# Kernel tuning notes

Measured on AMD Instinct MI355X. Metric: run time of the kernel, lower is better.

The kernel has to match this reference:

```python
import jax, jax.numpy as jnp
import numpy as np

B, T, H = 32, 4096, 128   # batch, seq len, feature dim (ctor L=128)
N = 128                    # S5 state size (S5(dim, dim))
DEPTH = 2                  # L_LT
D_OUT = 64                 # adaptive pool output length (ctor D)
LN_EPS = 1e-5


def setup_inputs() -> dict:
    key = jax.random.key(0)
    ks = iter(jax.random.split(key, 40))
    def nrm(shape, s):
        return (jax.random.normal(next(ks), shape, jnp.float32) * s).astype(jnp.float32)
    inp = {}
    inp['x'] = jax.random.normal(next(ks), (B, T, H), jnp.float32)
    # LayerNorm params (stacked over depth)
    inp['ln1_g'] = jnp.ones((DEPTH, H), jnp.float32)
    inp['ln1_b'] = jnp.zeros((DEPTH, H), jnp.float32)
    inp['ln2_g'] = jnp.ones((DEPTH, H), jnp.float32)
    inp['ln2_b'] = jnp.zeros((DEPTH, H), jnp.float32)
    # S5 params: diagonal complex Lambda, complex B/C, real D skip, per-state log step
    inp['Lam_re'] = -0.5 * jnp.ones((DEPTH, N), jnp.float32)
    inp['Lam_im'] = jnp.tile(jnp.pi * jnp.arange(N, dtype=jnp.float32), (DEPTH, 1))
    inp['B_re'] = nrm((DEPTH, N, H), 1.0 / np.sqrt(H))
    inp['B_im'] = nrm((DEPTH, N, H), 1.0 / np.sqrt(H))
    inp['C_re'] = nrm((DEPTH, H, N), 1.0 / np.sqrt(N))
    inp['C_im'] = nrm((DEPTH, H, N), 1.0 / np.sqrt(N))
    inp['D_skip'] = nrm((DEPTH, H), 1.0)
    inp['log_step'] = jax.random.uniform(next(ks), (DEPTH, N), jnp.float32,
                                         minval=np.log(1e-3), maxval=np.log(1e-1))
    # MLP params
    inp['W1'] = nrm((DEPTH, H, 2 * H), 1.0 / np.sqrt(H))
    inp['b1'] = jnp.zeros((DEPTH, 2 * H), jnp.float32)
    inp['W2'] = nrm((DEPTH, 2 * H, H), 1.0 / np.sqrt(2 * H))
    inp['b2'] = jnp.zeros((DEPTH, H), jnp.float32)
    # Conv1d params (out_ch, in_ch, k=5)
    cs = 1.0 / np.sqrt(H * 5)
    inp['conv1_w'] = nrm((H, H, 5), cs)
    inp['conv1_b'] = jnp.zeros((H,), jnp.float32)
    inp['conv2_w'] = nrm((H, H, 5), cs)
    inp['conv2_b'] = jnp.zeros((H,), jnp.float32)
    return inp


def _layer_norm(x, g, b):
    mu = jnp.mean(x, axis=-1, keepdims=True)
    var = jnp.mean(jnp.square(x - mu), axis=-1, keepdims=True)
    return (x - mu) * jax.lax.rsqrt(var + LN_EPS) * g + b


def _s5(u, lam_re, lam_im, b_re, b_im, c_re, c_im, d_skip, log_step):
    # u: [B, T, H] real. Diagonal S5 with ZOH discretization + parallel scan.
    lam = lam_re + 1j * lam_im                       # (N,) complex
    dt = jnp.exp(log_step)                           # (N,)
    lam_bar = jnp.exp(lam * dt)                      # (N,)
    Bc = b_re + 1j * b_im                            # (N, H)
    B_bar = ((lam_bar - 1.0) / lam)[:, None] * Bc    # (N, H)
    Bu = jnp.einsum('bth,nh->btn', u.astype(jnp.complex64), B_bar)  # [B,T,N]
    A = jnp.broadcast_to(lam_bar.astype(jnp.complex64), Bu.shape)
    def binop(e1, e2):
        a1, x1 = e1
        a2, x2 = e2
        return a1 * a2, a2 * x1 + x2
    _, xs = jax.lax.associative_scan(binop, (A, Bu), axis=1)        # [B,T,N]
    Cc = c_re + 1j * c_im                            # (H, N)
    y = 2.0 * jnp.real(jnp.einsum('btn,hn->bth', xs, Cc)) + u * d_skip
    return y


def _conv1d_s2(x, w, b):
    # x: [B, C, L]; stride 2, padding 2, kernel 5
    y = jax.lax.conv_general_dilated(x, w, window_strides=(2,), padding=[(2, 2)],
                                     dimension_numbers=('NCH', 'OIH', 'NCH'))
    return y + b[None, :, None]


def reference(x, ln1_g, ln1_b, ln2_g, ln2_b, Lam_re, Lam_im, B_re, B_im,
              C_re, C_im, D_skip, log_step, W1, b1, W2, b2,
              conv1_w, conv1_b, conv2_w, conv2_b):
    for i in range(DEPTH):
        # S5 sub-block
        res = x
        xn = _layer_norm(x, ln1_g[i], ln1_b[i])
        x = res + _s5(xn, Lam_re[i], Lam_im[i], B_re[i], B_im[i],
                      C_re[i], C_im[i], D_skip[i], log_step[i])
        # MLP sub-block (dropout = identity in eval)
        res = x
        xn = _layer_norm(x, ln2_g[i], ln2_b[i])
        h = jax.nn.gelu(jnp.einsum('bth,hf->btf', xn, W1[i]) + b1[i], approximate=False)
        x = res + jnp.einsum('btf,fh->bth', h, W2[i]) + b2[i]
    x = jnp.transpose(x, (0, 2, 1))                  # [B, H, T]
    x = jax.nn.relu(_conv1d_s2(x, conv1_w, conv1_b))  # [B, H, T/2]
    x = jax.nn.relu(_conv1d_s2(x, conv2_w, conv2_b))  # [B, H, T/4]
    Lin = x.shape[-1]
    # AdaptiveAvgPool1d(D_OUT): Lin divisible by D_OUT -> uniform windows
    x = x.reshape(x.shape[0], x.shape[1], D_OUT, Lin // D_OUT).mean(axis=-1)
    return x  # [B, H, D_OUT]
```

## Files before the change

kernel.cpp:

```cpp
#include <hip/hip_runtime.h>
#include <math.h>

#define BATCH 32
#define TSEQ  4096
#define HD    128
#define NST   128
#define BT    (BATCH*TSEQ)
#define LC    64
#define NCHK  (TSEQ/LC)

typedef unsigned short bf16;
typedef __attribute__((ext_vector_type(8))) short bf16x8;
typedef __attribute__((ext_vector_type(4))) float f32x4;

__device__ inline float bf2f(bf16 s) {
    union { unsigned int u; float f; } v; v.u = ((unsigned int)s) << 16; return v.f;
}
__device__ inline bf16 f2bf(float f) {
    union { float f; unsigned int u; } v; v.f = f;
    unsigned int u = v.u;
    unsigned int r = (u + 0x7fffu + ((u >> 16) & 1u)) >> 16;
    return (bf16)r;
}
__device__ inline unsigned int pkpair(float lo, float hi) {
    union { float f; unsigned int u; } a, b;
    a.f = lo; b.f = hi;
    return __builtin_amdgcn_perm(b.u + 0x8000u, a.u + 0x8000u, 0x07060302u);
}
__device__ inline bf16x8 pack8f(float4 f0, float4 f1) {
    union { bf16x8 v; unsigned int u[4]; } t;
    t.u[0] = pkpair(f0.x, f0.y);
    t.u[1] = pkpair(f0.z, f0.w);
    t.u[2] = pkpair(f1.x, f1.y);
    t.u[3] = pkpair(f1.z, f1.w);
    return t.v;
}
__device__ inline float2 cmul2(float2 a, float2 b) {
    return make_float2(a.x*b.x - a.y*b.y, a.x*b.y + a.y*b.x);
}
__device__ inline float gelu_f(float x) {
    float u = x*(0.7978845608f + 0.0356774081f*x*x);
    return __fdividef(x, 1.f + __expf(-2.f*u));
}
__device__ inline float2 upk(unsigned int w) {
    union { unsigned int u; float f; } a, b;
    a.u = w << 16; b.u = w & 0xffff0000u;
    return make_float2(a.f, b.f);
}
__device__ inline unsigned int pk(float2 x) { return pkpair(x.x, x.y); }

__global__ void prep_s5(const float* __restrict__ Lam_re, const float* __restrict__ Lam_im,
                        const float* __restrict__ B_re,  const float* __restrict__ B_im,
                        const float* __restrict__ C_re,  const float* __restrict__ C_im,
                        const float* __restrict__ log_step,
                        const float* __restrict__ ln1_g, const float* __restrict__ ln1_b,
                        const float* __restrict__ D_skip,
                        bf16* __restrict__ Wbu_bf,
                        bf16* __restrict__ Wc_bf,
                        float* __restrict__ Sb, float* __restrict__ biasb,
                        float* __restrict__ gd, float* __restrict__ bd,
                        float4* __restrict__ coefs,
                        float2* __restrict__ apow)
{
    int i = blockIdx.x, n = threadIdx.x;
    int in = i*NST + n;
    float lr = Lam_re[in], li = Lam_im[in];
    float dt = expf(log_step[in]);
    float ea = expf(lr*dt);
    float ar = ea*cosf(li*dt), ai = ea*sinf(li*dt);
    float xx = ar - 1.f, yy = ai;
    float den = lr*lr + li*li;
    float sr = (xx*lr + yy*li)/den;
    float si = (yy*lr - xx*li)/den;
    float2 a2 = make_float2(ar, ai);
    float2 p = a2;
    float2* apr = apow + (size_t)i*64*128;
    for (int j = 0; j < 64; ++j) {
        apr[n*64 + j] = p;
        p = cmul2(p, a2);
    }
    float2 q = a2;
    #pragma unroll
    for (int t = 0; t < 6; ++t) q = cmul2(q, q);
    coefs[in] = make_float4(ar, ai, q.x, q.y);

    const float* g  = ln1_g + i*HD;
    const float* bb = ln1_b + i*HD;
    const float* br = B_re + (size_t)in*HD;
    const float* bi = B_im + (size_t)in*HD;
    bf16* wb = Wbu_bf + (size_t)i*256*128;
    float s_re = 0.f, s_im = 0.f, bc_re = 0.f, bc_im = 0.f;
    for (int h = 0; h < HD; ++h) {
        float wre = sr*br[h] - si*bi[h];
        float wim = sr*bi[h] + si*br[h];
        bf16 wrb = f2bf(g[h]*wre), wib = f2bf(g[h]*wim);
        wb[(2*n)*128 + h]   = wrb;
        wb[(2*n+1)*128 + h] = wib;
        s_re += bf2f(wrb); s_im += bf2f(wib);
        bc_re += bb[h]*wre; bc_im += bb[h]*wim;
    }
    Sb[i*256 + 2*n] = s_re;     Sb[i*256 + 2*n+1] = s_im;
    biasb[i*256 + 2*n] = bc_re; biasb[i*256 + 2*n+1] = bc_im;

    const float* cr = C_re + (size_t)i*HD*NST;
    const float* ci = C_im + (size_t)i*HD*NST;
    bf16* wc = Wc_bf + (size_t)i*128*256;
    for (int h = 0; h < HD; ++h) {
        wc[h*256 + 2*n]   = f2bf( 2.f * cr[h*NST + n]);
        wc[h*256 + 2*n+1] = f2bf(-2.f * ci[h*NST + n]);
    }
    gd[i*HD + n] = g[n]*D_skip[i*HD + n];
    bd[i*HD + n] = bb[n]*D_skip[i*HD + n];
}

__global__ void prep_w1(const float* __restrict__ W1, const float* __restrict__ b1,
                        const float* __restrict__ ln2_g, const float* __restrict__ ln2_b,
                        bf16* __restrict__ W1_bf, float* __restrict__ S1,
                        float* __restrict__ bias1p)
{
    int i = blockIdx.x, f = threadIdx.x;
    const float* g  = ln2_g + i*HD;
    const float* bb = ln2_b + i*HD;
    bf16* w = W1_bf + (size_t)i*256*128;
    int j = ((f >> 5) << 5) | (((f >> 2) & 1) << 4) | (((f >> 3) & 3) << 2) | (f & 3);
    float S = 0.f, bi_ = b1[i*256 + f];
    for (int h = 0; h < HD; ++h) {
        float wv = W1[(size_t)i*32768 + h*256 + f];
        bf16 wbv = f2bf(g[h]*wv);
        w[j*128 + h] = wbv;
        S += bf2f(wbv);
        bi_ += bb[h]*wv;
    }
    S1[i*256 + f] = S;
    bias1p[i*256 + f] = bi_;
}

__global__ void prep_w2(const float* __restrict__ W2, bf16* __restrict__ W2_bf)
{
    int i = blockIdx.x, h = threadIdx.x;
    bf16* w = W2_bf + (size_t)i*128*256;
    for (int f = 0; f < 256; ++f)
        w[h*256 + f] = f2bf(W2[(size_t)i*32768 + f*128 + h]);
}

__global__ void prep_wB(const float* __restrict__ w1, const float* __restrict__ w2,
                        bf16* __restrict__ wB1, bf16* __restrict__ wB2)
{
    int idx = blockIdx.x*256 + threadIdx.x;
    if (idx >= 163840) return;
    const float* w = (idx < 81920) ? w1 : w2;
    bf16* wb       = (idx < 81920) ? wB1 : wB2;
    int r   = idx % 81920;
    int c   = r / 640;
    int tap = (r % 640) / 128;
    int ic  = r % 128;
    wb[r] = f2bf(w[(c*128 + ic)*5 + tap]);
}

template<typename TA>
__global__ __launch_bounds__(512, 2) void lngemm2(
    const TA* __restrict__ A,
    const bf16* __restrict__ Bt,
    const float* __restrict__ Svec, const float* __restrict__ bvec,
    bf16* __restrict__ outB,
    float2* __restrict__ munrs)
{
    __shared__ bf16 Bs[256*136];
    __shared__ float Sl[256], bl[256];

    int tid = threadIdx.x;
    #pragma unroll
    for (int it = 0; it < 8; ++it) {
        int f = it*512 + tid;
        int n = f >> 4, kk = (f & 15)*8;
        *(bf16x8*)&Bs[n*136 + kk] = *(const bf16x8*)(Bt + n*128 + kk);
    }
    if (tid < 256) { Sl[tid] = Svec[tid]; bl[tid] = bvec[tid]; }
    __syncthreads();

    int wid = tid >> 6, lane = tid & 63;
    int quad = lane >> 4, cl = lane & 15;
    int s0 = blockIdx.x*16 + wid*2;
    size_t row0 = (size_t)s0*16 + cl;

    bf16x8 af[2][4];
    float mu[2], rs[2], mr[2];
    #pragma unroll
    for (int p = 0; p < 2; ++p) {
        size_t row = row0 + (size_t)p*16;
        float sm = 0.f, sq = 0.f;
        if constexpr (sizeof(TA) == 2) {
            const bf16* ar = (const bf16*)A + row*128;
            #pragma unroll
            for (int ks = 0; ks < 4; ++ks) {
                af[p][ks] = *(const bf16x8*)(ar + quad*8 + ks*32);
                union { bf16x8 v; unsigned int u[4]; } aa; aa.v = af[p][ks];
                #pragma unroll
                for (int jp = 0; jp < 4; ++jp) {
                    float2 vv = upk(aa.u[jp]);
                    sm += vv.x + vv.y;
                    sq += vv.x*vv.x + vv.y*vv.y;
                }
            }
        } else {
            const float* ar = (const float*)A + row*128;
            #pragma unroll
            for (int ks = 0; ks < 4; ++ks) {
                float4 f0 = *(const float4*)(ar + quad*8 + ks*32);
                float4 f1 = *(const float4*)(ar + quad*8 + ks*32 + 4);
                sm += f0.x + f0.y + f0.z + f0.w + f1.x + f1.y + f1.z + f1.w;
                sq += f0.x*f0.x + f0.y*f0.y + f0.z*f0.z + f0.w*f0.w
                    + f1.x*f1.x + f1.y*f1.y + f1.z*f1.z + f1.w*f1.w;
                af[p][ks] = pack8f(f0, f1);
            }
        }
        sm += __shfl_xor(sm, 16); sm += __shfl_xor(sm, 32);
        sq += __shfl_xor(sq, 16); sq += __shfl_xor(sq, 32);
        mu[p] = sm * (1.f/128.f);
        rs[p] = rsqrtf(sq*(1.f/128.f) - mu[p]*mu[p] + 1e-5f);
        mr[p] = mu[p]*rs[p];
        if (quad == 0) munrs[row] = make_float2(mu[p], rs[p]);
    }

    #pragma unroll
    for (int g = 0; g < 4; ++g) {
        f32x4 acc0[4] = {}, acc1[4] = {};
        #pragma unroll
        for (int t4 = 0; t4 < 4; ++t4) {
            const bf16* wrp = &Bs[(((g*4+t4)*16) + cl)*136 + quad*8];
            #pragma unroll
            for (int ks = 0; ks < 4; ++ks) {
                bf16x8 w = *(const bf16x8*)(wrp + ks*32);
                acc0[t4] = __builtin_amdgcn_mfma_f32_16x16x32_bf16(w, af[0][ks], acc0[t4], 0, 0, 0);
                acc1[t4] = __builtin_amdgcn_mfma_f32_16x16x32_bf16(w, af[1][ks], acc1[t4], 0, 0, 0);
            }
        }
        #pragma unroll
        for (int t4 = 0; t4 < 4; ++t4) {
            int n0 = (g*4+t4)*16 + quad*4;
            float4 S4 = *(const float4*)&Sl[n0];
            float4 b4 = *(const float4*)&bl[n0];
            float4 o;
            o.x = rs[0]*acc0[t4][0] - mr[0]*S4.x + b4.x;
            o.y = rs[0]*acc0[t4][1] - mr[0]*S4.y + b4.y;
            o.z = rs[0]*acc0[t4][2] - mr[0]*S4.z + b4.z;
            o.w = rs[0]*acc0[t4][3] - mr[0]*S4.w + b4.w;
            *(uint2*)(outB + row0*256 + n0) = make_uint2(pkpair(o.x, o.y), pkpair(o.z, o.w));
            o.x = rs[1]*acc1[t4][0] - mr[1]*S4.x + b4.x;
            o.y = rs[1]*acc1[t4][1] - mr[1]*S4.y + b4.y;
            o.z = rs[1]*acc1[t4][2] - mr[1]*S4.z + b4.z;
            o.w = rs[1]*acc1[t4][3] - mr[1]*S4.w + b4.w;
            *(uint2*)(outB + (row0+16)*256 + n0) = make_uint2(pkpair(o.x, o.y), pkpair(o.z, o.w));
        }
    }
}

template<typename TR>
__global__ __launch_bounds__(512, 2) void gemm2s(
    const bf16* __restrict__ A,
    const bf16* __restrict__ Bt,
    bf16* out,
    const TR* resid,
    const float2* __restrict__ munrs,
    const float* __restrict__ gdp, const float* __restrict__ bdp,
    const float2* __restrict__ carry,
    const float2* __restrict__ apow)
{
    __shared__ bf16 Bs[128*264];
    __shared__ float gdl[128], bdl[128];

    int tid = threadIdx.x;
    #pragma unroll
    for (int it = 0; it < 8; ++it) {
        int f = it*512 + tid;
        int n = f >> 5, kk = (f & 31)*8;
        *(bf16x8*)&Bs[n*264 + kk] = *(const bf16x8*)(Bt + n*256 + kk);
    }
    if (tid < 128) { gdl[tid] = gdp[tid]; bdl[tid] = bdp[tid]; }
    __syncthreads();

    int wid = tid >> 6, lane = tid & 63;
    int quad = lane >> 4, cl = lane & 15;
    int s0 = blockIdx.x*16 + wid*2;
    size_t row0 = (size_t)s0*16 + cl;

    bf16x8 af[2][8];
    float mu[2], rs[2];
    #pragma unroll
    for (int p = 0; p < 2; ++p) {
        size_t row = row0 + (size_t)p*16;
        float2 m2 = munrs[row]; mu[p] = m2.x; rs[p] = m2.y;
        const bf16* ar = A + row*256 + quad*8;
        int b  = (int)(row >> 12);
        int tp = (int)(row & 4095);
        int cc = tp >> 6, j = tp & 63;
        const float2* cin = carry + (size_t)cc*(BATCH*NST) + (size_t)b*NST;
        const float2* ap  = apow + j;
        #pragma unroll
        for (int ks = 0; ks < 8; ++ks) {
            union { bf16x8 v; unsigned int u[4]; } t;
            t.v = *(const bf16x8*)(ar + ks*32);
            int n0 = quad*4 + ks*16;
            #pragma unroll
            for (int jp = 0; jp < 4; ++jp) {
                float2 v  = upk(t.u[jp]);
                float2 ad = cmul2(ap[(size_t)(n0+jp)*64], cin[n0+jp]);
                t.u[jp] = pk(make_float2(v.x + ad.x, v.y + ad.y));
            }
            af[p][ks] = t.v;
        }
    }

    ushort4 rvh[2][8];
    if constexpr (sizeof(TR) == 2) {
        #pragma unroll
        for (int p = 0; p < 2; ++p)
            #pragma unroll
            for (int nt = 0; nt < 8; ++nt)
                rvh[p][nt] = *(const ushort4*)((const bf16*)resid
                               + (row0 + (size_t)p*16)*128 + nt*16 + quad*4);
    }

    #pragma unroll
    for (int nt = 0; nt < 8; ++nt) {
        const bf16* wrp = &Bs[(nt*16 + cl)*264 + quad*8];
        f32x4 a0 = {}, a1 = {};
        #pragma unroll
        for (int ks = 0; ks < 8; ++ks) {
            bf16x8 w = *(const bf16x8*)(wrp + ks*32);
            a0 = __builtin_amdgcn_mfma_f32_16x16x32_bf16(w, af[0][ks], a0, 0, 0, 0);
            a1 = __builtin_amdgcn_mfma_f32_16x16x32_bf16(w, af[1][ks], a1, 0, 0, 0);
        }
        int n0 = nt*16 + quad*4;
        float4 g4 = *(const float4*)&gdl[n0];
        float4 b4 = *(const float4*)&bdl[n0];
        #pragma unroll
        for (int p = 0; p < 2; ++p) {
            f32x4 ac = p ? a1 : a0;
            size_t oidx = (row0 + (size_t)p*16)*128 + n0;
            float4 rv;
            if constexpr (sizeof(TR) == 2) {
                ushort4 u4 = rvh[p][nt];
                rv = make_float4(bf2f(u4.x), bf2f(u4.y), bf2f(u4.z), bf2f(u4.w));
            } else {
                rv = *(const float4*)((const float*)resid + oidx);
            }
            float4 o;
            o.x = rv.x + ac[0] + (rv.x - mu[p])*rs[p]*g4.x + b4.x;
            o.y = rv.y + ac[1] + (rv.y - mu[p])*rs[p]*g4.y + b4.y;
            o.z = rv.z + ac[2] + (rv.z - mu[p])*rs[p]*g4.z + b4.z;
            o.w = rv.w + ac[3] + (rv.w - mu[p])*rs[p]*g4.w + b4.w;
            *(uint2*)(out + oidx) = make_uint2(pkpair(o.x, o.y), pkpair(o.z, o.w));
        }
    }
}

__global__ __launch_bounds__(1024, 2) void mlp_fused(
    const bf16* X,
    const bf16* __restrict__ W1t,
    const bf16* __restrict__ W2t,
    const float* __restrict__ S1v, const float* __restrict__ b1v,
    const float* __restrict__ b2v,
    bf16* out)
{
    __shared__ bf16 As1[256*136];
    __shared__ bf16 Bs2[128*264];
    __shared__ float S1l[256], b1l[256], b2l[128];

    int tid = threadIdx.x;
    #pragma unroll
    for (int it = 0; it < 4; ++it) {
        int f = it*1024 + tid;
        int n = f >> 4, kk = (f & 15)*8;
        *(bf16x8*)&As1[n*136 + kk] = *(const bf16x8*)(W1t + n*128 + kk);
    }
    #pragma unroll
    for (int it = 0; it < 4; ++it) {
        int f = it*1024 + tid;
        int n = f >> 5, kk = (f & 31)*8;
        *(bf16x8*)&Bs2[n*264 + kk] = *(const bf16x8*)(W2t + n*256 + kk);
    }
    if (tid < 256)      { S1l[tid] = S1v[tid]; b1l[tid] = b1v[tid]; }
    else if (tid < 384) { int h = tid - 256; b2l[h] = b2v[h]; }
    __syncthreads();

    int wid = tid >> 6, lane = tid & 63;
    int quad = lane >> 4, cl = lane & 15;
    int s = blockIdx.x*16 + wid;
    size_t row = (size_t)s*16 + cl;

    const bf16* ar = X + row*128;
    bf16x8 af[4];
    float sm = 0.f, sq = 0.f;
    #pragma unroll
    for (int ks = 0; ks < 4; ++ks) {
        af[ks] = *(const bf16x8*)(ar + quad*8 + ks*32);
        union { bf16x8 v; unsigned int u[4]; } aa; aa.v = af[ks];
        #pragma unroll
        for (int jp = 0; jp < 4; ++jp) {
            float2 vv = upk(aa.u[jp]);
            sm += vv.x + vv.y;
            sq += vv.x*vv.x + vv.y*vv.y;
        }
    }
    sm += __shfl_xor(sm, 16); sm += __shfl_xor(sm, 32);
    sq += __shfl_xor(sq, 16); sq += __shfl_xor(sq, 32);
    float mu = sm * (1.f/128.f);
    float rs = rsqrtf(sq*(1.f/128.f) - mu*mu + 1e-5f);
    float mr = mu*rs;

    union { unsigned int u[16][2]; bf16x8 v[8]; } hp;
    #pragma unroll
    for (int half = 0; half < 2; ++half) {
        f32x4 acc[8] = {};
        #pragma unroll
        for (int nt = 0; nt < 8; ++nt) {
            const bf16* wrp = &As1[(((half*8+nt)*16) + cl)*136 + quad*8];
            #pragma unroll
            for (int ks = 0; ks < 4; ++ks)
                acc[nt] = __builtin_amdgcn_mfma_f32_16x16x32_bf16(
                              *(const bf16x8*)(wrp + ks*32), af[ks], acc[nt], 0, 0, 0);
        }
        #pragma unroll
        for (int nt = 0; nt < 8; ++nt) {
            int NT = half*8 + nt;
            int fb = ((NT >> 1) << 5) + (quad << 3) + ((NT & 1) << 2);
            float4 S4 = *(const float4*)&S1l[fb];
            float4 b4 = *(const float4*)&b1l[fb];
            float4 o;
            o.x = gelu_f(rs*acc[nt][0] - mr*S4.x + b4.x);
            o.y = gelu_f(rs*acc[nt][1] - mr*S4.y + b4.y);
            o.z = gelu_f(rs*acc[nt][2] - mr*S4.z + b4.z);
            o.w = gelu_f(rs*acc[nt][3] - mr*S4.w + b4.w);
            hp.u[NT][0] = pkpair(o.x, o.y);
            hp.u[NT][1] = pkpair(o.z, o.w);
        }
    }

    #pragma unroll
    for (int nt = 0; nt < 8; ++nt) {
        const bf16* wrp = &Bs2[(nt*16 + cl)*264 + quad*8];
        f32x4 a0 = {};
        #pragma unroll
        for (int ks = 0; ks < 8; ++ks) {
            bf16x8 w = *(const bf16x8*)(wrp + ks*32);
            a0 = __builtin_amdgcn_mfma_f32_16x16x32_bf16(w, hp.v[ks], a0, 0, 0, 0);
        }
        int n0 = nt*16 + quad*4;
        size_t oidx = row*128 + n0;
        float4 b4 = *(const float4*)&b2l[n0];
        ushort4 u4 = *(const ushort4*)(X + oidx);
        float4 o;
        o.x = a0[0] + b4.x + bf2f(u4.x);
        o.y = a0[1] + b4.y + bf2f(u4.y);
        o.z = a0[2] + b4.z + bf2f(u4.z);
        o.w = a0[3] + b4.w + bf2f(u4.w);
        *(uint2*)(out + oidx) = make_uint2(pkpair(o.x, o.y), pkpair(o.z, o.w));
    }
}

__global__ __launch_bounds__(256) void scan_local(uint2* __restrict__ xs,
                                                  const float4* __restrict__ coefs,
                                                  float2* __restrict__ carry)
{
    int flat = blockIdx.x*256 + threadIdx.x;
    int n2 = flat & 63;
    int b = (flat >> 6) & 31;
    int c = flat >> 11;
    float4 cf0 = coefs[2*n2], cf1 = coefs[2*n2+1];
    float2 a0 = make_float2(cf0.x, cf0.y);
    float2 a1 = make_float2(cf1.x, cf1.y);
    uint2* base = xs + ((size_t)(b*TSEQ + c*LC))*64 + n2;
    float2 x0 = make_float2(0.f, 0.f), x1 = make_float2(0.f, 0.f);
    uint2 v = base[0];
    #pragma unroll 4
    for (int j = 0; j < LC; ++j) {
        uint2 vc = v;
        if (j + 1 < LC) v = base[(size_t)(j+1)*64];
        float2 v0 = upk(vc.x), v1 = upk(vc.y);
        x0 = make_float2(a0.x*x0.x - a0.y*x0.y + v0.x, a0.x*x0.y + a0.y*x0.x + v0.y);
        x1 = make_float2(a1.x*x1.x - a1.y*x1.y + v1.x, a1.x*x1.y + a1.y*x1.x + v1.y);
        base[(size_t)j*64] = make_uint2(pk(x0), pk(x1));
    }
    carry[c*(BATCH*NST) + b*NST + 2*n2]   = x0;
    carry[c*(BATCH*NST) + b*NST + 2*n2+1] = x1;
}

__global__ void scan_carry(float2* __restrict__ carry, const float4* __restrict__ coefs)
{
    int flat = blockIdx.x*256 + threadIdx.x;
    int n = flat & 127;
    float4 cf = coefs[n];
    float2 aL = make_float2(cf.z, cf.w);
    float2 x = make_float2(0.f, 0.f);
    for (int c = 0; c < NCHK; ++c) {
        float2* p = carry + c*(BATCH*NST) + flat;
        float2 v = *p;
        *p = x;
        x = make_float2(aL.x*x.x - aL.y*x.y + v.x, aL.x*x.y + aL.y*x.x + v.y);
    }
}

__global__ __launch_bounds__(256, 4) void conv1_mfma(
    const bf16* __restrict__ X,
    const bf16* __restrict__ wB,
    const float* __restrict__ bias,
    bf16* __restrict__ out,
    int Tin, int Lout)
{
    __shared__ bf16 As[128][72];
    __shared__ bf16 Bs[128][72];
    int tid  = threadIdx.x;
    int lane = tid & 63;
    int wave = tid >> 6;
    int wm = wave >> 1, wn = wave & 1;
    int quad = lane >> 4, cl = lane & 15;
    int row0 = blockIdx.x * 128;
    int b  = row0 / Lout;
    int l0 = row0 % Lout;
    const bf16* Xb = X + (size_t)b*Tin*128;

    f32x4 acc[4][4] = {};

    for (int k0 = 0; k0 < 640; k0 += 64) {
        int tap = k0 / 128;
        int icb = k0 % 128;
        #pragma unroll
        for (int it = 0; it < 4; ++it) {
            int idx = it*256 + tid;
            int r = idx >> 3, kof = (idx & 7) * 8;
            int t = 2*(l0 + r) - 2 + tap;
            bf16x8 z = {0,0,0,0,0,0,0,0};
            if (t >= 0 && t < Tin) z = *(const bf16x8*)(Xb + (size_t)t*128 + icb + kof);
            *(bf16x8*)&As[r][kof] = z;
        }
        #pragma unroll
        for (int it = 0; it < 4; ++it) {
            int idx = it*256 + tid;
            int n = idx >> 3, kof = (idx & 7) * 8;
            *(bf16x8*)&Bs[n][kof] = *(const bf16x8*)(wB + (size_t)n*640 + k0 + kof);
        }
        __syncthreads();
        #pragma unroll
        for (int kk = 0; kk < 64; kk += 32) {
            bf16x8 af[4], bfr[4];
            #pragma unroll
            for (int i = 0; i < 4; ++i)
                af[i] = *(const bf16x8*)&As[wm*64 + i*16 + cl][kk + quad*8];
            #pragma unroll
            for (int j = 0; j < 4; ++j)
                bfr[j] = *(const bf16x8*)&Bs[wn*64 + j*16 + cl][kk + quad*8];
            #pragma unroll
            for (int i = 0; i < 4; ++i)
                #pragma unroll
                for (int j = 0; j < 4; ++j)
                    acc[i][j] = __builtin_amdgcn_mfma_f32_16x16x32_bf16(
                                    bfr[j], af[i], acc[i][j], 0, 0, 0);
        }
        __syncthreads();
    }

    #pragma unroll
    for (int i = 0; i < 4; ++i) {
        int grow = row0 + wm*64 + i*16 + cl;
        #pragma unroll
        for (int j = 0; j < 4; ++j) {
            int gcol = wn*64 + j*16 + quad*4;
            float4 bv = *(const float4*)(bias + gcol);
            float4 t;
            t.x = fmaxf(acc[i][j][0] + bv.x, 0.f); t.y = fmaxf(acc[i][j][1] + bv.y, 0.f);
            t.z = fmaxf(acc[i][j][2] + bv.z, 0.f); t.w = fmaxf(acc[i][j][3] + bv.w, 0.f);
            uint2 pu = make_uint2(pkpair(t.x, t.y), pkpair(t.z, t.w));
            *(uint2*)(out + (size_t)grow*128 + gcol) = pu;
        }
    }
}

__global__ __launch_bounds__(256, 4) void conv2_pool(
    const bf16* __restrict__ X,
    const bf16* __restrict__ wB,
    const float* __restrict__ bias,
    float* __restrict__ outp,
    int Tin, int Lout)
{
    __shared__ bf16 As[128][72];
    __shared__ bf16 Bs[128][72];
    int tid  = threadIdx.x;
    int lane = tid & 63;
    int wave = tid >> 6;
    int wm = wave >> 1, wn = wave & 1;
    int quad = lane >> 4, cl = lane & 15;
    int row0 = blockIdx.x * 128;
    int b  = row0 / Lout;
    int l0 = row0 % Lout;
    int d0 = l0 / 16;
    const bf16* Xb = X + (size_t)b*Tin*128;

    f32x4 acc[4][4] = {};

    for (int k0 = 0; k0 < 640; k0 += 64) {
        int tap = k0 / 128;
        int icb = k0 % 128;
        #pragma unroll
        for (int it = 0; it < 4; ++it) {
            int idx = it*256 + tid;
            int r = idx >> 3, kof = (idx & 7) * 8;
            int t = 2*(l0 + r) - 2 + tap;
            bf16x8 z = {0,0,0,0,0,0,0,0};
            if (t >= 0 && t < Tin) z = *(const bf16x8*)(Xb + (size_t)t*128 + icb + kof);
            *(bf16x8*)&As[r][kof] = z;
        }
        #pragma unroll
        for (int it = 0; it < 4; ++it) {
            int idx = it*256 + tid;
            int n = idx >> 3, kof = (idx & 7) * 8;
            *(bf16x8*)&Bs[n][kof] = *(const bf16x8*)(wB + (size_t)n*640 + k0 + kof);
        }
        __syncthreads();
        #pragma unroll
        for (int kk = 0; kk < 64; kk += 32) {
            bf16x8 af[4], bfr[4];
            #pragma unroll
            for (int i = 0; i < 4; ++i)
                af[i] = *(const bf16x8*)&As[wm*64 + i*16 + cl][kk + quad*8];
            #pragma unroll
            for (int j = 0; j < 4; ++j)
                bfr[j] = *(const bf16x8*)&Bs[wn*64 + j*16 + cl][kk + quad*8];
            #pragma unroll
            for (int i = 0; i < 4; ++i)
                #pragma unroll
                for (int j = 0; j < 4; ++j)
                    acc[i][j] = __builtin_amdgcn_mfma_f32_16x16x32_bf16(
                                    bfr[j], af[i], acc[i][j], 0, 0, 0);
        }
        __syncthreads();
    }

    #pragma unroll
    for (int j = 0; j < 4; ++j) {
        int gcol = wn*64 + j*16 + quad*4;
        float4 bv = *(const float4*)(bias + gcol);
        #pragma unroll
        for (int i = 0; i < 4; ++i) {
            float4 sp;
            sp.x = fmaxf(acc[i][j][0] + bv.x, 0.f);
            sp.y = fmaxf(acc[i][j][1] + bv.y, 0.f);
            sp.z = fmaxf(acc[i][j][2] + bv.z, 0.f);
            sp.w = fmaxf(acc[i][j][3] + bv.w, 0.f);
            #pragma unroll
            for (int off = 1; off <= 8; off <<= 1) {
                sp.x += __shfl_xor(sp.x, off);
                sp.y += __shfl_xor(sp.y, off);
                sp.z += __shfl_xor(sp.z, off);
                sp.w += __shfl_xor(sp.w, off);
            }
            if (cl == 0) {
                int d = d0 + wm*4 + i;
                float* op = outp + (size_t)b*8192 + (size_t)gcol*64 + d;
                op[0]   = sp.x * (1.f/16.f);
                op[64]  = sp.y * (1.f/16.f);
                op[128] = sp.z * (1.f/16.f);
                op[192] = sp.w * (1.f/16.f);
            }
        }
    }
}

extern "C" void kernel_launch(void* const* d_in, const int* in_sizes, int n_in,
                              void* d_out, int out_size, void* d_ws, size_t ws_size,
                              hipStream_t stream)
{
    (void)in_sizes; (void)n_in; (void)out_size; (void)ws_size;
    const float* x_in    = (const float*)d_in[0];
    const float* ln1_g   = (const float*)d_in[1];
    const float* ln1_b   = (const float*)d_in[2];
    const float* ln2_g   = (const float*)d_in[3];
    const float* ln2_b   = (const float*)d_in[4];
    const float* Lam_re  = (const float*)d_in[5];
    const float* Lam_im  = (const float*)d_in[6];
    const float* B_re    = (const float*)d_in[7];
    const float* B_im    = (const float*)d_in[8];
    const float* C_re    = (const float*)d_in[9];
    const float* C_im    = (const float*)d_in[10];
    const float* D_skip  = (const float*)d_in[11];
    const float* log_step= (const float*)d_in[12];
    const float* W1      = (const float*)d_in[13];
    const float* b1      = (const float*)d_in[14];
    const float* W2      = (const float*)d_in[15];
    const float* b2      = (const float*)d_in[16];
    const float* conv1_w = (const float*)d_in[17];
    const float* conv1_b = (const float*)d_in[18];
    const float* conv2_w = (const float*)d_in[19];
    const float* conv2_b = (const float*)d_in[20];
    float* out = (float*)d_out;

    char* ws = (char*)d_ws;
    bf16*   Xbf    = (bf16*) (ws);
    bf16*   Cbuf   = (bf16*) (ws + (size_t)33554432);
    bf16*   Cv1    = (bf16*) (ws + (size_t)100663296);
    float2* munrs  = (float2*)(ws + (size_t)117440512);
    char*   wreg   = ws + (size_t)118489088;
    bf16*   Wbu_bf = (bf16*)(wreg);
    bf16*   Wc_bf  = (bf16*)(wreg + 131072);
    bf16*   W1_bf  = (bf16*)(wreg + 262144);
    bf16*   W2_bf  = (bf16*)(wreg + 393216);
    float*  Sb     = (float*)(wreg + 524288);
    float*  biasb  = (float*)(wreg + 526336);
    float*  S1     = (float*)(wreg + 528384);
    float*  bias1p = (float*)(wreg + 530432);
    float*  gd     = (float*)(wreg + 532480);
    float*  bd     = (float*)(wreg + 533504);
    float4* coefs  = (float4*)(wreg + 534528);
    bf16*   wB1    = (bf16*)(wreg + 538624);
    bf16*   wB2    = (bf16*)(wreg + 702464);
    float2* carry  = (float2*)(wreg + 866304);
    float2* apow   = (float2*)(wreg + 2963456);

    prep_s5<<<2, 128, 0, stream>>>(Lam_re, Lam_im, B_re, B_im, C_re, C_im, log_step,
                                   ln1_g, ln1_b, D_skip,
                                   Wbu_bf, Wc_bf, Sb, biasb, gd, bd, coefs, apow);
    prep_w1<<<2, 256, 0, stream>>>(W1, b1, ln2_g, ln2_b, W1_bf, S1, bias1p);
    prep_w2<<<2, 128, 0, stream>>>(W2, W2_bf);
    prep_wB<<<640, 256, 0, stream>>>(conv1_w, conv2_w, wB1, wB2);

    for (int i = 0; i < 2; ++i) {
        if (i == 0)
            lngemm2<float><<<512, 512, 0, stream>>>(
                x_in, Wbu_bf, Sb, biasb, Cbuf, munrs);
        else
            lngemm2<bf16><<<512, 512, 0, stream>>>(
                Xbf, Wbu_bf + 32768, Sb + 256, biasb + 256, Cbuf, munrs);
        scan_local<<<512, 256, 0, stream>>>((uint2*)Cbuf, coefs + i*NST, carry);
        scan_carry<<<16, 256, 0, stream>>>(carry, coefs + i*NST);
        if (i == 0)
            gemm2s<float><<<512, 512, 0, stream>>>(
                Cbuf, Wc_bf, Xbf, x_in, munrs, gd, bd, carry, apow);
        else
            gemm2s<bf16><<<512, 512, 0, stream>>>(
                Cbuf, Wc_bf + 32768, Xbf, Xbf, munrs, gd + 128, bd + 128,
                carry, apow + 64*128);
        mlp_fused<<<512, 1024, 0, stream>>>(
            Xbf, W1_bf + (size_t)i*32768, W2_bf + (size_t)i*32768,
            S1 + i*256, bias1p + i*256, b2 + i*HD, Xbf);
    }

    conv1_mfma<<<512, 256, 0, stream>>>(Xbf, wB1, conv1_b, Cv1, 4096, 2048);
    conv2_pool<<<256, 256, 0, stream>>>(Cv1, wB2, conv2_b, out, 2048, 1024);
}
```

Before: 521.1 us.

## Process two row tiles per warp in MLP kernel and share one LDS weight buffer

The fused MLP kernel now runs 512 threads per block. Each wave handles two 16-row tiles, so every weight fragment read from LDS feeds two MFMAs. W1 and W2 now share a single LDS buffer: W2 is loaded into it only after the first GEMM finishes, with extra barriers around the reload. Residual reads are issued early, before the second GEMM. This cuts LDS size and LDS reads per MFMA, at the cost of more registers, serialized W2 staging, and the risk of lower occupancy.

```diff
diff --git a/kernel.cpp b/kernel.cpp
--- a/kernel.cpp
+++ b/kernel.cpp
@@ -355,7 +355,7 @@
     }
 }
 
-__global__ __launch_bounds__(1024, 2) void mlp_fused(
+__global__ __launch_bounds__(512, 2) void mlp_fused(
     const bf16* X,
     const bf16* __restrict__ W1t,
     const bf16* __restrict__ W2t,
@@ -363,99 +363,124 @@
     const float* __restrict__ b2v,
     bf16* out)
 {
-    __shared__ bf16 As1[256*136];
-    __shared__ bf16 Bs2[128*264];
+    __shared__ bf16 Wl[256*136];
     __shared__ float S1l[256], b1l[256], b2l[128];
 
     int tid = threadIdx.x;
     #pragma unroll
-    for (int it = 0; it < 4; ++it) {
-        int f = it*1024 + tid;
+    for (int it = 0; it < 8; ++it) {
+        int f = it*512 + tid;
         int n = f >> 4, kk = (f & 15)*8;
-        *(bf16x8*)&As1[n*136 + kk] = *(const bf16x8*)(W1t + n*128 + kk);
-    }
-    #pragma unroll
-    for (int it = 0; it < 4; ++it) {
-        int f = it*1024 + tid;
-        int n = f >> 5, kk = (f & 31)*8;
-        *(bf16x8*)&Bs2[n*264 + kk] = *(const bf16x8*)(W2t + n*256 + kk);
+        *(bf16x8*)&Wl[n*136 + kk] = *(const bf16x8*)(W1t + n*128 + kk);
     }
     if (tid < 256)      { S1l[tid] = S1v[tid]; b1l[tid] = b1v[tid]; }
-    else if (tid < 384) { int h = tid - 256; b2l[h] = b2v[h]; }
+    else if (tid < 384) { b2l[tid-256] = b2v[tid-256]; }
     __syncthreads();
 
     int wid = tid >> 6, lane = tid & 63;
     int quad = lane >> 4, cl = lane & 15;
-    int s = blockIdx.x*16 + wid;
-    size_t row = (size_t)s*16 + cl;
-
-    const bf16* ar = X + row*128;
-    bf16x8 af[4];
-    float sm = 0.f, sq = 0.f;
-    #pragma unroll
-    for (int ks = 0; ks < 4; ++ks) {
-        af[ks] = *(const bf16x8*)(ar + quad*8 + ks*32);
-        union { bf16x8 v; unsigned int u[4]; } aa; aa.v = af[ks];
-        #pragma unroll
-        for (int jp = 0; jp < 4; ++jp) {
-            float2 vv = upk(aa.u[jp]);
-            sm += vv.x + vv.y;
-            sq += vv.x*vv.x + vv.y*vv.y;
-        }
-    }
-    sm += __shfl_xor(sm, 16); sm += __shfl_xor(sm, 32);
-    sq += __shfl_xor(sq, 16); sq += __shfl_xor(sq, 32);
-    float mu = sm * (1.f/128.f);
-    float rs = rsqrtf(sq*(1.f/128.f) - mu*mu + 1e-5f);
-    float mr = mu*rs;
-
-    union { unsigned int u[16][2]; bf16x8 v[8]; } hp;
-    #pragma unroll
-    for (int half = 0; half < 2; ++half) {
-        f32x4 acc[8] = {};
-        #pragma unroll
-        for (int nt = 0; nt < 8; ++nt) {
-            const bf16* wrp = &As1[(((half*8+nt)*16) + cl)*136 + quad*8];
-            #pragma unroll
-            for (int ks = 0; ks < 4; ++ks)
-                acc[nt] = __builtin_amdgcn_mfma_f32_16x16x32_bf16(
-                              *(const bf16x8*)(wrp + ks*32), af[ks], acc[nt], 0, 0, 0);
-        }
-        #pragma unroll
-        for (int nt = 0; nt < 8; ++nt) {
-            int NT = half*8 + nt;
-            int fb = ((NT >> 1) << 5) + (quad << 3) + ((NT & 1) << 2);
-            float4 S4 = *(const float4*)&S1l[fb];
-            float4 b4 = *(const float4*)&b1l[fb];
+    int s0 = blockIdx.x*16 + wid*2;
+    size_t row0 = (size_t)s0*16 + cl;
+
+    bf16x8 af[2][4];
+    float mu[2], rs[2], mr[2];
+    #pragma unroll
+    for (int p = 0; p < 2; ++p) {
+        size_t row = row0 + (size_t)p*16;
+        const bf16* ar = X + row*128;
+        float sm = 0.f, sq = 0.f;
+        #pragma unroll
+        for (int ks = 0; ks < 4; ++ks) {
+            af[p][ks] = *(const bf16x8*)(ar + quad*8 + ks*32);
+            union { bf16x8 v; unsigned int u[4]; } aa; aa.v = af[p][ks];
+            #pragma unroll
+            for (int jp = 0; jp < 4; ++jp) {
+                float2 vv = upk(aa.u[jp]);
+                sm += vv.x + vv.y;
+                sq += vv.x*vv.x + vv.y*vv.y;
+            }
+        }
+        sm += __shfl_xor(sm, 16); sm += __shfl_xor(sm, 32);
+        sq += __shfl_xor(sq, 16); sq += __shfl_xor(sq, 32);
+        mu[p] = sm * (1.f/128.f);
+        rs[p] = rsqrtf(sq*(1.f/128.f) - mu[p]*mu[p] + 1e-5f);
+        mr[p] = mu[p]*rs[p];
+    }
+
+    union HP { unsigned int u[16][2]; bf16x8 v[8]; };
+    HP hp[2];
+    #pragma unroll
+    for (int NT = 0; NT < 16; ++NT) {
+        const bf16* wrp = &Wl[((NT*16) + cl)*136 + quad*8];
+        f32x4 a0 = {}, a1 = {};
+        #pragma unroll
+        for (int ks = 0; ks < 4; ++ks) {
+            bf16x8 w = *(const bf16x8*)(wrp + ks*32);
+            a0 = __builtin_amdgcn_mfma_f32_16x16x32_bf16(w, af[0][ks], a0, 0, 0, 0);
+            a1 = __builtin_amdgcn_mfma_f32_16x16x32_bf16(w, af[1][ks], a1, 0, 0, 0);
+        }
+        int fb = ((NT >> 1) << 5) + (quad << 3) + ((NT & 1) << 2);
+        float4 S4 = *(const float4*)&S1l[fb];
+        float4 b4 = *(const float4*)&b1l[fb];
+        #pragma unroll
+        for (int p = 0; p < 2; ++p) {
+            f32x4 ac = p ? a1 : a0;
             float4 o;
-            o.x = gelu_f(rs*acc[nt][0] - mr*S4.x + b4.x);
-            o.y = gelu_f(rs*acc[nt][1] - mr*S4.y + b4.y);
-            o.z = gelu_f(rs*acc[nt][2] - mr*S4.z + b4.z);
-            o.w = gelu_f(rs*acc[nt][3] - mr*S4.w + b4.w);
-            hp.u[NT][0] = pkpair(o.x, o.y);
-            hp.u[NT][1] = pkpair(o.z, o.w);
-        }
-    }
+            o.x = gelu_f(rs[p]*ac[0] - mr[p]*S4.x + b4.x);
+            o.y = gelu_f(rs[p]*ac[1] - mr[p]*S4.y + b4.y);
+            o.z = gelu_f(rs[p]*ac[2] - mr[p]*S4.z + b4.z);
+            o.w = gelu_f(rs[p]*ac[3] - mr[p]*S4.w + b4.w);
+            hp[p].u[NT][0] = pkpair(o.x, o.y);
+            hp[p].u[NT][1] = pkpair(o.z, o.w);
+        }
+    }
+
+    __syncthreads();
+
+    bf16x8 w2r[8];
+    #pragma unroll
+    for (int it = 0; it < 8; ++it) {
+        int f = it*512 + tid;
+        w2r[it] = *(const bf16x8*)(W2t + (size_t)(f >> 5)*256 + (f & 31)*8);
+    }
+    #pragma unroll
+    for (int it = 0; it < 8; ++it) {
+        int f = it*512 + tid;
+        *(bf16x8*)&Wl[(f >> 5)*264 + (f & 31)*8] = w2r[it];
+    }
+    __syncthreads();
+
+    ushort4 rvh[2][8];
+    #pragma unroll
+    for (int p = 0; p < 2; ++p)
+        #pragma unroll
+        for (int nt = 0; nt < 8; ++nt)
+            rvh[p][nt] = *(const ushort4*)(X + (row0 + (size_t)p*16)*128 + nt*16 + quad*4);
 
     #pragma unroll
     for (int nt = 0; nt < 8; ++nt) {
-        const bf16* wrp = &Bs2[(nt*16 + cl)*264 + quad*8];
-        f32x4 a0 = {};
+        const bf16* wrp = &Wl[(nt*16 + cl)*264 + quad*8];
+        f32x4 a0 = {}, a1 = {};
         #pragma unroll
         for (int ks = 0; ks < 8; ++ks) {
             bf16x8 w = *(const bf16x8*)(wrp + ks*32);
-            a0 = __builtin_amdgcn_mfma_f32_16x16x32_bf16(w, hp.v[ks], a0, 0, 0, 0);
+            a0 = __builtin_amdgcn_mfma_f32_16x16x32_bf16(w, hp[0].v[ks], a0, 0, 0, 0);
+            a1 = __builtin_amdgcn_mfma_f32_16x16x32_bf16(w, hp[1].v[ks], a1, 0, 0, 0);
         }
         int n0 = nt*16 + quad*4;
-        size_t oidx = row*128 + n0;
         float4 b4 = *(const float4*)&b2l[n0];
-        ushort4 u4 = *(const ushort4*)(X + oidx);
-        float4 o;
-        o.x = a0[0] + b4.x + bf2f(u4.x);
-        o.y = a0[1] + b4.y + bf2f(u4.y);
-        o.z = a0[2] + b4.z + bf2f(u4.z);
-        o.w = a0[3] + b4.w + bf2f(u4.w);
-        *(uint2*)(out + oidx) = make_uint2(pkpair(o.x, o.y), pkpair(o.z, o.w));
+        #pragma unroll
+        for (int p = 0; p < 2; ++p) {
+            f32x4 ac = p ? a1 : a0;
+            size_t oidx = (row0 + (size_t)p*16)*128 + n0;
+            ushort4 u4 = rvh[p][nt];
+            float4 o;
+            o.x = ac[0] + b4.x + bf2f(u4.x);
+            o.y = ac[1] + b4.y + bf2f(u4.y);
+            o.z = ac[2] + b4.z + bf2f(u4.z);
+            o.w = ac[3] + b4.w + bf2f(u4.w);
+            *(uint2*)(out + oidx) = make_uint2(pkpair(o.x, o.y), pkpair(o.z, o.w));
+        }
     }
 }
 
@@ -739,7 +764,7 @@
             gemm2s<bf16><<<512, 512, 0, stream>>>(
                 Cbuf, Wc_bf + 32768, Xbf, Xbf, munrs, gd + 128, bd + 128,
                 carry, apow + 64*128);
-        mlp_fused<<<512, 1024, 0, stream>>>(
+        mlp_fused<<<512, 512, 0, stream>>>(
             Xbf, W1_bf + (size_t)i*32768, W2_bf + (size_t)i*32768,
             S1 + i*256, bias1p + i*256, b2 + i*HD, Xbf);
     }
```

Result: slower. 589.7 us (+13.2%).
